# Kernel tuning notes

Hardware: AMD Instinct MI355X
Metric: run time of the kernel (lower is better)

Reference implementation:

```python
import jax, jax.numpy as jnp
import numpy as np

B, N = 2048, 110
H1, F1 = 5, 24   # gat1: 5 heads, 24-dim, concat
H2, F2 = 3, 3    # gat2: 3 heads, 3-dim, average
NEG = -9e15
ALPHA = 0.2  # tf.nn.leaky_relu default alpha


def _glorot(key, shape):
    fan_in, fan_out = shape[-2], shape[-1]
    lim = np.sqrt(6.0 / (fan_in + fan_out))
    return jax.random.uniform(key, shape, jnp.float32, -lim, lim)


def setup_inputs() -> dict:
    key = jax.random.key(0)
    ks = jax.random.split(key, 12)
    X = jax.random.normal(ks[0], (B, N, N), jnp.float32)
    # sparse-ish 0/1 adjacency with self-loops
    A = (jax.random.uniform(ks[1], (B, N, N)) < 0.3).astype(jnp.float32)
    A = jnp.maximum(A, jnp.eye(N, dtype=jnp.float32)[None])
    return {
        "X": X,
        "A": A,
        "M": jax.random.normal(ks[2], (N, N), jnp.float32),  # learnable mask
        "W1": _glorot(ks[3], (H1, N, F1)),
        "as1": _glorot(ks[4], (H1, F1, 1))[..., 0],
        "an1": _glorot(ks[5], (H1, F1, 1))[..., 0],
        "b1": jnp.zeros((F1,), jnp.float32),
        "W2": _glorot(ks[6], (H2, H1 * F1, F2)),
        "as2": _glorot(ks[7], (H2, F2, 1))[..., 0],
        "an2": _glorot(ks[8], (H2, F2, 1))[..., 0],
        "b2": jnp.zeros((F2,), jnp.float32),
        "fc1_w": _glorot(ks[9], (F2, 1)),
        "fc2_w": _glorot(ks[10], (N, N)),
    }


def _gat_layer(X, A, W, a_s, a_n, b, concat):
    # X: [B,N,Din]; W: [H,Din,F]; a_s,a_n: [H,F]; b: [F]
    feats = jnp.einsum('bni,hif->bhnf', X, W)               # per-head projection
    e_s = jnp.einsum('bhnf,hf->bhn', feats, a_s)
    e_n = jnp.einsum('bhnf,hf->bhn', feats, a_n)
    e = jax.nn.leaky_relu(e_s[..., :, None] + e_n[..., None, :], ALPHA)  # [B,H,N,N]
    e = jnp.where(A[:, None] > 0.0, e, NEG)                  # adjacency mask
    attn = jax.nn.softmax(e, axis=-1)
    h = jnp.einsum('bhnm,bhmf->bhnf', attn, feats) + b       # aggregate + bias
    if concat:
        h = jax.nn.leaky_relu(h, ALPHA)
        b_, hh, n_, f_ = h.shape
        return h.transpose(0, 2, 1, 3).reshape(b_, n_, hh * f_)
    # 'average': add heads / H, then activation
    return jax.nn.leaky_relu(h.mean(axis=1), ALPHA)


def reference(X, A, M, W1, as1, an1, b1, W2, as2, an2, b2, fc1_w, fc2_w):
    Xm = X * jax.nn.sigmoid(M)[None]                         # learnable mask gating
    h1 = _gat_layer(Xm, A, W1, as1, an1, b1, concat=True)    # [B,N,H1*F1]
    h2 = _gat_layer(h1, A, W2, as2, an2, b2, concat=False)   # [B,N,F2]
    node_prob = jax.nn.sigmoid(h2 @ fc1_w)                   # [B,N,1]
    t = node_prob.reshape(-1, N)                             # [B,N]
    attn_prob = jax.nn.softmax(t @ fc2_w, axis=-1)           # [B,N]
    return jnp.sum(t * attn_prob, axis=1, keepdims=True)     # [B,1]
```

## Files before the change

kernel.cpp:

```cpp
#include <hip/hip_runtime.h>
#include <math.h>

#define NB 2048
#define NV 110
#define NH1 5
#define NF1 24
#define NH2 3
#define NF2 3
#define C1 (NH1*NF1)
#define LALPHA 0.2f

constexpr int NN = NV*NV;
constexpr int T1 = 512;
constexpr int KP = 136;
constexpr int W1ROWS = 144;

typedef _Float16 f16;
typedef f16  f16x8 __attribute__((ext_vector_type(8)));
typedef f16  f16x4 __attribute__((ext_vector_type(4)));
typedef __fp16 h16x2 __attribute__((ext_vector_type(2)));
typedef float f32x4 __attribute__((ext_vector_type(4)));

__device__ __forceinline__ f32x4 mfma16(f16x8 a, f16x8 b, f32x4 c) {
  return __builtin_amdgcn_mfma_f32_16x16x32_f16(a, b, c, 0, 0, 0);
}
__device__ __forceinline__ float lrelu(float x){ return x > 0.f ? x : LALPHA*x; }
__device__ __forceinline__ float frcp(float x){ return __builtin_amdgcn_rcpf(x); }
__device__ __forceinline__ float sigm(float x){ return frcp(1.f+__expf(-x)); }
__device__ __forceinline__ float expm4(float v){
  return __builtin_amdgcn_exp2f(fmaf(v, 1.442695041f, -5.770780163f));
}
__device__ __forceinline__ float wmax(float v){
  #pragma unroll
  for (int d=32; d; d>>=1) v = fmaxf(v, __shfl_xor(v,d));
  return v;
}
__device__ __forceinline__ float wsum(float v){
  #pragma unroll
  for (int d=32; d; d>>=1) v += __shfl_xor(v,d);
  return v;
}
__device__ __forceinline__ f32x4 ld4u(const float* p){
  f32x4 v; __builtin_memcpy(&v, p, 16); return v;
}

__global__ void precomp_kernel(const float* __restrict__ M, const float* __restrict__ W1,
                               const float* __restrict__ as1, const float* __restrict__ an1,
                               const float* __restrict__ W2, const float* __restrict__ as2,
                               const float* __restrict__ an2, const float* __restrict__ fc2w,
                               float* __restrict__ Msig, f16* __restrict__ W1tg,
                               f16* __restrict__ W2tg, f16* __restrict__ fc2tg) {
  const int i = blockIdx.x*256 + threadIdx.x;
  if (i < NN) {
    Msig[i] = sigm(M[i]);
  } else if (i < NN + W1ROWS*KP) {
    const int j = i - NN, f = j/KP, k = j%KP;
    float v = 0.f;
    if (k < NV) {
      if (f < C1) {
        v = W1[(f/NF1)*(NV*NF1) + k*NF1 + (f%NF1)];
      } else if (f >= 128 && f < 133) {
        const int h = f - 128;
        for (int ff = 0; ff < NF1; ++ff)
          v += W1[h*(NV*NF1) + k*NF1 + ff] * as1[h*NF1 + ff];
      } else if (f >= 133 && f < 138) {
        const int h = f - 133;
        for (int ff = 0; ff < NF1; ++ff)
          v += W1[h*(NV*NF1) + k*NF1 + ff] * an1[h*NF1 + ff];
      }
    }
    W1tg[f*KP + k] = (f16)v;
  } else if (i < NN + W1ROWS*KP + 16*KP) {
    const int j = i - NN - W1ROWS*KP, r = j/KP, k = j%KP;
    float v = 0.f;
    if (k < C1) {
      if (r < 9) {
        v = W2[(r/NF2)*(C1*NF2) + k*NF2 + (r%NF2)];
      } else if (r < 12) {
        const int g = r - 9;
        for (int f2 = 0; f2 < NF2; ++f2)
          v += W2[g*(C1*NF2) + k*NF2 + f2] * as2[g*NF2 + f2];
      } else if (r < 15) {
        const int g = r - 12;
        for (int f2 = 0; f2 < NF2; ++f2)
          v += W2[g*(C1*NF2) + k*NF2 + f2] * an2[g*NF2 + f2];
      }
    }
    W2tg[r*KP + k] = (f16)v;
  } else if (i < NN + W1ROWS*KP + 16*KP + 112*KP) {
    const int j = i - NN - W1ROWS*KP - 16*KP, col = j/KP, k = j%KP;
    float v = 0.f;
    if (col < NV && k < NV) v = fc2w[k*NV + col];
    fc2tg[col*KP + k] = (f16)v;
  }
}

__global__ __launch_bounds__(T1, 4) void gat_fused(
  const float* __restrict__ X, const float* __restrict__ A,
  const float* __restrict__ Msig, const f16* __restrict__ W1tg,
  const float* __restrict__ b1,  const f16* __restrict__ W2tg,
  const float* __restrict__ b2,  const float* __restrict__ fc1w,
  const f16* __restrict__ fc2tg, float* __restrict__ out)
{
  __shared__ __attribute__((aligned(16))) f16 sXm [112*KP];
  __shared__ __attribute__((aligned(16))) f16 sFt [128*KP];
  __shared__ __attribute__((aligned(16))) f16 sF2t[16*KP];
  __shared__ __attribute__((aligned(16))) float sES [NH1*112];
  __shared__ __attribute__((aligned(16))) float sEN [NH1*128];
  __shared__ __attribute__((aligned(16))) float sES2[NH2*112];
  __shared__ __attribute__((aligned(16))) float sEN2[NH2*128];
  __shared__ unsigned long long sAM[2*112];
  __shared__ __attribute__((aligned(16))) float sROW [112];
  __shared__ __attribute__((aligned(16))) float sROW2[3*112];

  const int b = blockIdx.x, tid = threadIdx.x;
  const int wv = tid >> 6, lane = tid & 63;
  const int lr = lane & 15, lh = lane >> 4;
  const float* __restrict__ Xb = X + (size_t)b*NN;
  const float* __restrict__ Ab = A + (size_t)b*NN;

  float* const sT = sES;
  float* const sS = sES + 112;
  f16*   const t16 = sF2t;

  for (int n = tid; n < 110; n += T1) {
    *(unsigned*)&sXm[n*KP + 110] = 0u;
    *(uint4*)&sXm[n*KP + 112] = uint4{0,0,0,0};
    *(uint4*)&sXm[n*KP + 120] = uint4{0,0,0,0};
    *(uint4*)&sXm[n*KP + 128] = uint4{0,0,0,0};
  }
  for (int i = tid; i < 2*KP/8; i += T1)
    ((uint4*)&sXm[110*KP])[i] = uint4{0,0,0,0};
  for (int n = tid; n < 128; n += T1) {
    *(uint4*)&sFt[n*KP + 112] = uint4{0,0,0,0};
    *(uint4*)&sFt[n*KP + 120] = uint4{0,0,0,0};
    *(uint4*)&sFt[n*KP + 128] = uint4{0,0,0,0};
  }
  for (int i = tid; i < (16*KP)/8; i += T1)
    ((uint4*)sF2t)[i] = uint4{0,0,0,0};
  if (tid < 4) sAM[220 + tid] = 0ull;

  for (int t = tid; t < NV*28; t += T1) {
    const int n = t/28, c = t%28, k = 4*c;
    if (c < 27) {
      f32x4 x = ld4u(Xb + n*NV + k);
      f32x4 m = ld4u(Msig + n*NV + k);
      union { f16x4 v4; h16x2 h2[2]; } u;
      u.h2[0] = __builtin_amdgcn_cvt_pkrtz(x[0]*m[0], x[1]*m[1]);
      u.h2[1] = __builtin_amdgcn_cvt_pkrtz(x[2]*m[2], x[3]*m[3]);
      *(f16x4*)&sXm[n*KP + k] = u.v4;
    } else {
      sXm[n*KP + 108] = (f16)(Xb[n*NV+108]*Msig[n*NV+108]);
      sXm[n*KP + 109] = (f16)(Xb[n*NV+109]*Msig[n*NV+109]);
    }
  }
  #pragma unroll
  for (int i = 0; i < 14; ++i) {
    const int n = wv + 8*i;
    if (n < NV) {
      unsigned long long m0 = __ballot(Ab[n*NV + lane] > 0.f);
      const int mm = 64 + lane;
      unsigned long long m1 = __ballot((mm < NV) && (Ab[n*NV + mm] > 0.f));
      if (lane == 0) { sAM[2*n] = m0; sAM[2*n+1] = m1; }
    }
  }
  f16x8 bW[4], bL[4];
  #pragma unroll
  for (int k = 0; k < 4; ++k)
    bW[k] = *(const f16x8*)&W1tg[(wv*16 + lr)*KP + k*32 + lh*8];
  if (wv < 2) {
    #pragma unroll
    for (int k = 0; k < 4; ++k)
      bL[k] = *(const f16x8*)&W1tg[(128 + lr)*KP + k*32 + lh*8];
  }
  __syncthreads();

  #pragma unroll
  for (int m = 0; m < 7; ++m) {
    f32x4 acc = {0.f,0.f,0.f,0.f};
    #pragma unroll
    for (int k = 0; k < 4; ++k) {
      f16x8 af = *(const f16x8*)&sXm[(m*16 + lr)*KP + k*32 + lh*8];
      acc = mfma16(af, bW[k], acc);
    }
    f16x4 v;
    #pragma unroll
    for (int r = 0; r < 4; ++r) v[r] = (f16)acc[r];
    *(f16x4*)&sFt[(wv*16 + lr)*KP + m*16 + lh*4] = v;
  }
  if (wv < 2) {
    const int mlo = wv ? 4 : 0, mhi = wv ? 7 : 4;
    for (int m = mlo; m < mhi; ++m) {
      f32x4 acc = {0.f,0.f,0.f,0.f};
      #pragma unroll
      for (int k = 0; k < 4; ++k) {
        f16x8 af = *(const f16x8*)&sXm[(m*16 + lr)*KP + k*32 + lh*8];
        acc = mfma16(af, bL[k], acc);
      }
      const int mg0 = m*16 + lh*4;
      if (lr < 5)       *(f32x4*)&sES[lr*112 + mg0] = acc;
      else if (lr < 10) *(f32x4*)&sEN[(lr-5)*128 + mg0] = acc;
    }
  }
  __syncthreads();

  const int row  = wv*16 + lr;
  const int arow = (row < 112) ? row : 0;
  const unsigned long long am0 = sAM[2*arow], am1 = sAM[2*arow+1];
  const float bvt0 = (lr < NF1) ? b1[lr] : 0.f;
  const float bvt1 = (16 + lr < NF1) ? b1[16 + lr] : 0.f;

  f16 h1r[5][2][4];
  f16x8 pa[4];
  if (wv < 7) {
    #pragma unroll
    for (int p = 0; p < 5; ++p) {
      const float es = sES[p*112 + row];
      float psum = 0.f;
      #pragma unroll
      for (int k = 0; k < 4; ++k) {
        const int cb = k*32 + lh*8;
        const f32x4 enA = *(const f32x4*)&sEN[p*128 + cb];
        const f32x4 enB = *(const f32x4*)&sEN[p*128 + cb + 4];
        const unsigned bits = (unsigned)(((cb & 64) ? am1 : am0) >> (cb & 63)) & 0xFFu;
        float e[8];
        #pragma unroll
        for (int j = 0; j < 8; ++j) {
          float v = es + ((j < 4) ? enA[j] : enB[j-4]);
          v = fmaxf(v, LALPHA*v);
          v = (bits & (1u << j)) ? v : -1e30f;
          e[j] = expm4(v);
          psum += e[j];
        }
        union { f16x8 v8; h16x2 h2[4]; } u;
        u.h2[0] = __builtin_amdgcn_cvt_pkrtz(e[0], e[1]);
        u.h2[1] = __builtin_amdgcn_cvt_pkrtz(e[2], e[3]);
        u.h2[2] = __builtin_amdgcn_cvt_pkrtz(e[4], e[5]);
        u.h2[3] = __builtin_amdgcn_cvt_pkrtz(e[6], e[7]);
        pa[k] = u.v8;
      }
      psum += __shfl_xor(psum, 16);
      psum += __shfl_xor(psum, 32);
      if (lh == 0) sROW[row] = psum;
      #pragma unroll
      for (int nt2 = 0; nt2 < 2; ++nt2) {
        f32x4 acc = {0.f,0.f,0.f,0.f};
        #pragma unroll
        for (int k = 0; k < 4; ++k) {
          f16x8 bf = *(const f16x8*)&sFt[(p*NF1 + nt2*16 + lr)*KP + k*32 + lh*8];
          acc = mfma16(pa[k], bf, acc);
        }
        const f32x4 rs = *(const f32x4*)&sROW[wv*16 + lh*4];
        const float bv = nt2 ? bvt1 : bvt0;
        #pragma unroll
        for (int r = 0; r < 4; ++r)
          h1r[p][nt2][r] = (f16)lrelu(acc[r]*frcp(rs[r]) + bv);
      }
    }
    #pragma unroll
    for (int p = 0; p < 5; ++p) {
      #pragma unroll
      for (int nt2 = 0; nt2 < 2; ++nt2) {
        const int fl = nt2*16 + lr;
        if (fl < NF1) {
          #pragma unroll
          for (int r = 0; r < 4; ++r) {
            const int mg = wv*16 + lh*4 + r;
            if (mg < NV) sXm[mg*KP + p*NF1 + fl] = h1r[p][nt2][r];
          }
        }
      }
    }
    {
      f32x4 acc = {0.f,0.f,0.f,0.f};
      #pragma unroll
      for (int k = 0; k < 4; ++k) {
        f16x8 af = *(const f16x8*)&sXm[(wv*16 + lr)*KP + k*32 + lh*8];
        f16x8 bf = *(const f16x8*)&W2tg[lr*KP + k*32 + lh*8];
        acc = mfma16(af, bf, acc);
      }
      const int mg0 = wv*16 + lh*4;
      if (lr < 9) {
        #pragma unroll
        for (int r = 0; r < 4; ++r) {
          const int mg = mg0 + r;
          if (mg < NV) sF2t[lr*KP + mg] = (f16)acc[r];
        }
      } else if (lr < 12) {
        *(f32x4*)&sES2[(lr-9)*112 + mg0] = acc;
      } else if (lr < 15) {
        *(f32x4*)&sEN2[(lr-12)*128 + mg0] = acc;
      }
    }
  }
  __syncthreads();

  f32x4 a2_0 = {0.f,0.f,0.f,0.f};
  f32x4 a2_1 = {0.f,0.f,0.f,0.f};
  f32x4 a2_2 = {0.f,0.f,0.f,0.f};
  if (wv < 7) {
    #pragma unroll
    for (int g = 0; g < 3; ++g) {
      const float es = sES2[g*112 + row];
      float psum = 0.f;
      #pragma unroll
      for (int k = 0; k < 4; ++k) {
        const int cb = k*32 + lh*8;
        const f32x4 enA = *(const f32x4*)&sEN2[g*128 + cb];
        const f32x4 enB = *(const f32x4*)&sEN2[g*128 + cb + 4];
        const unsigned bits = (unsigned)(((cb & 64) ? am1 : am0) >> (cb & 63)) & 0xFFu;
        float e[8];
        #pragma unroll
        for (int j = 0; j < 8; ++j) {
          float v = es + ((j < 4) ? enA[j] : enB[j-4]);
          v = fmaxf(v, LALPHA*v);
          v = (bits & (1u << j)) ? v : -1e30f;
          e[j] = expm4(v);
          psum += e[j];
        }
        union { f16x8 v8; h16x2 h2[4]; } u;
        u.h2[0] = __builtin_amdgcn_cvt_pkrtz(e[0], e[1]);
        u.h2[1] = __builtin_amdgcn_cvt_pkrtz(e[2], e[3]);
        u.h2[2] = __builtin_amdgcn_cvt_pkrtz(e[4], e[5]);
        u.h2[3] = __builtin_amdgcn_cvt_pkrtz(e[6], e[7]);
        pa[k] = u.v8;
      }
      psum += __shfl_xor(psum, 16);
      psum += __shfl_xor(psum, 32);
      if (lh == 0) sROW2[g*112 + row] = psum;
      const int brow = (lr < NF2) ? (g*NF2 + lr) : 15;
      #pragma unroll
      for (int k = 0; k < 4; ++k) {
        f16x8 bf = *(const f16x8*)&sF2t[brow*KP + k*32 + lh*8];
        if (g == 0)      a2_0 = mfma16(pa[k], bf, a2_0);
        else if (g == 1) a2_1 = mfma16(pa[k], bf, a2_1);
        else             a2_2 = mfma16(pa[k], bf, a2_2);
      }
    }
    const int mg0 = wv*16 + lh*4;
    const float fcv = (lr < NF2) ? fc1w[lr] : 0.f;
    const float b2v = (lr < NF2) ? b2[lr]  : 0.f;
    const f32x4 rs0 = *(const f32x4*)&sROW2[0*112 + mg0];
    const f32x4 rs1 = *(const f32x4*)&sROW2[1*112 + mg0];
    const f32x4 rs2 = *(const f32x4*)&sROW2[2*112 + mg0];
    #pragma unroll
    for (int r = 0; r < 4; ++r) {
      const float hsum = a2_0[r]*frcp(rs0[r]) + a2_1[r]*frcp(rs1[r])
                       + a2_2[r]*frcp(rs2[r]);
      float hv = (lr < NF2) ? lrelu(hsum*(1.f/NH2) + b2v)*fcv : 0.f;
      hv += __shfl_xor(hv, 1);
      hv += __shfl_xor(hv, 2);
      hv += __shfl_xor(hv, 4);
      hv += __shfl_xor(hv, 8);
      if (lr == 0) {
        const int mg = mg0 + r;
        if (mg < NV) sT[mg] = sigm(hv);
      }
    }
  }
  __syncthreads();
  for (int i = tid; i < 16*KP; i += T1) {
    const int k = i % KP;
    t16[i] = (k < NV) ? (f16)sT[k] : (f16)0.f;
  }
  __syncthreads();
  if (wv < 7) {
    f32x4 acc = {0.f,0.f,0.f,0.f};
    #pragma unroll
    for (int k = 0; k < 4; ++k) {
      f16x8 af = *(const f16x8*)&t16[lr*KP + k*32 + lh*8];
      f16x8 bf = *(const f16x8*)&fc2tg[(wv*16 + lr)*KP + k*32 + lh*8];
      acc = mfma16(af, bf, acc);
    }
    const int col = wv*16 + lr;
    if (lh == 0 && col < NV) sS[col] = acc[0];
  }
  __syncthreads();
  if (wv == 0) {
    const float s0 = sS[lane];
    const float s1 = (64+lane < NV) ? sS[64+lane] : -1e38f;
    const float mx = wmax(fmaxf(s0, s1));
    const float p0 = __expf(s0 - mx);
    const float p1 = (64+lane < NV) ? __expf(s1 - mx) : 0.f;
    const float sum = wsum(p0 + p1);
    float val = sT[lane]*p0 + ((64+lane < NV) ? sT[64+lane]*p1 : 0.f);
    val = wsum(val);
    if (lane == 0) out[b] = val*frcp(sum);
  }
}

extern "C" void kernel_launch(void* const* d_in, const int* in_sizes, int n_in,
                              void* d_out, int out_size, void* d_ws, size_t ws_size,
                              hipStream_t stream) {
  const float* X   = (const float*)d_in[0];
  const float* A   = (const float*)d_in[1];
  const float* M   = (const float*)d_in[2];
  const float* W1  = (const float*)d_in[3];
  const float* as1 = (const float*)d_in[4];
  const float* an1 = (const float*)d_in[5];
  const float* b1  = (const float*)d_in[6];
  const float* W2  = (const float*)d_in[7];
  const float* as2 = (const float*)d_in[8];
  const float* an2 = (const float*)d_in[9];
  const float* b2  = (const float*)d_in[10];
  const float* fc1 = (const float*)d_in[11];
  const float* fc2 = (const float*)d_in[12];
  float* out = (float*)d_out;

  float* Msig = (float*)d_ws;
  f16* W1tg  = (f16*)((char*)d_ws + 48400);
  f16* W2tg  = (f16*)((char*)d_ws + 48400 + W1ROWS*KP*2);
  f16* fc2tg = (f16*)((char*)d_ws + 48400 + W1ROWS*KP*2 + 16*KP*2);

  const int pre_items = NN + W1ROWS*KP + 16*KP + 112*KP;
  precomp_kernel<<<(pre_items + 255)/256, 256, 0, stream>>>(
      M, W1, as1, an1, W2, as2, an2, fc2, Msig, W1tg, W2tg, fc2tg);
  gat_fused<<<NB, T1, 0, stream>>>(X, A, Msig, W1tg, b1, W2tg,
                                   b2, fc1, fc2tg, out);
}
```

Before: 148.8 us.

## Make GAT kernel persistent and prefetch next batch's inputs during layer 2

Launches a fixed grid of 512 blocks that each loop over four graphs instead of one block per graph. Staging of the next graph's X and adjacency into shared memory is moved after layer-1 completes, so its global loads overlap the layer-2 attention and final readout. The attention-logit projection is also spread across seven waves instead of two, and per-block constants are hoisted out of the loop. This trades fewer resident blocks and possibly less latency hiding across blocks for reuse of setup work and overlap of loads with compute.

```diff
diff --git a/kernel.cpp b/kernel.cpp
--- a/kernel.cpp
+++ b/kernel.cpp
@@ -12,6 +12,8 @@
 
 constexpr int NN = NV*NV;
 constexpr int T1 = 512;
+constexpr int GRID = 512;
+constexpr int ITERS = NB/GRID;
 constexpr int KP = 136;
 constexpr int W1ROWS = 144;
 
@@ -113,15 +115,42 @@
   __shared__ __attribute__((aligned(16))) float sROW [112];
   __shared__ __attribute__((aligned(16))) float sROW2[3*112];
 
-  const int b = blockIdx.x, tid = threadIdx.x;
+  const int tid = threadIdx.x;
   const int wv = tid >> 6, lane = tid & 63;
   const int lr = lane & 15, lh = lane >> 4;
-  const float* __restrict__ Xb = X + (size_t)b*NN;
-  const float* __restrict__ Ab = A + (size_t)b*NN;
 
   float* const sT = sES;
   float* const sS = sES + 112;
   f16*   const t16 = sF2t;
+
+  auto stage_xm = [&](const float* __restrict__ Xb) {
+    for (int t = tid; t < NV*28; t += T1) {
+      const int n = t/28, c = t%28, k = 4*c;
+      if (c < 27) {
+        f32x4 x = ld4u(Xb + n*NV + k);
+        f32x4 m = ld4u(Msig + n*NV + k);
+        union { f16x4 v4; h16x2 h2[2]; } u;
+        u.h2[0] = __builtin_amdgcn_cvt_pkrtz(x[0]*m[0], x[1]*m[1]);
+        u.h2[1] = __builtin_amdgcn_cvt_pkrtz(x[2]*m[2], x[3]*m[3]);
+        *(f16x4*)&sXm[n*KP + k] = u.v4;
+      } else {
+        sXm[n*KP + 108] = (f16)(Xb[n*NV+108]*Msig[n*NV+108]);
+        sXm[n*KP + 109] = (f16)(Xb[n*NV+109]*Msig[n*NV+109]);
+      }
+    }
+  };
+  auto stage_am = [&](const float* __restrict__ Ab) {
+    #pragma unroll
+    for (int i = 0; i < 14; ++i) {
+      const int n = wv + 8*i;
+      if (n < NV) {
+        unsigned long long m0 = __ballot(Ab[n*NV + lane] > 0.f);
+        const int mm = 64 + lane;
+        unsigned long long m1 = __ballot((mm < NV) && (Ab[n*NV + mm] > 0.f));
+        if (lane == 0) { sAM[2*n] = m0; sAM[2*n+1] = m1; }
+      }
+    }
+  };
 
   for (int n = tid; n < 110; n += T1) {
     *(unsigned*)&sXm[n*KP + 110] = 0u;
@@ -140,252 +169,248 @@
     ((uint4*)sF2t)[i] = uint4{0,0,0,0};
   if (tid < 4) sAM[220 + tid] = 0ull;
 
-  for (int t = tid; t < NV*28; t += T1) {
-    const int n = t/28, c = t%28, k = 4*c;
-    if (c < 27) {
-      f32x4 x = ld4u(Xb + n*NV + k);
-      f32x4 m = ld4u(Msig + n*NV + k);
-      union { f16x4 v4; h16x2 h2[2]; } u;
-      u.h2[0] = __builtin_amdgcn_cvt_pkrtz(x[0]*m[0], x[1]*m[1]);
-      u.h2[1] = __builtin_amdgcn_cvt_pkrtz(x[2]*m[2], x[3]*m[3]);
-      *(f16x4*)&sXm[n*KP + k] = u.v4;
-    } else {
-      sXm[n*KP + 108] = (f16)(Xb[n*NV+108]*Msig[n*NV+108]);
-      sXm[n*KP + 109] = (f16)(Xb[n*NV+109]*Msig[n*NV+109]);
-    }
-  }
-  #pragma unroll
-  for (int i = 0; i < 14; ++i) {
-    const int n = wv + 8*i;
-    if (n < NV) {
-      unsigned long long m0 = __ballot(Ab[n*NV + lane] > 0.f);
-      const int mm = 64 + lane;
-      unsigned long long m1 = __ballot((mm < NV) && (Ab[n*NV + mm] > 0.f));
-      if (lane == 0) { sAM[2*n] = m0; sAM[2*n+1] = m1; }
-    }
-  }
+  stage_xm(X + (size_t)blockIdx.x*NN);
+  stage_am(A + (size_t)blockIdx.x*NN);
+
   f16x8 bW[4], bL[4];
   #pragma unroll
   for (int k = 0; k < 4; ++k)
     bW[k] = *(const f16x8*)&W1tg[(wv*16 + lr)*KP + k*32 + lh*8];
-  if (wv < 2) {
+  if (wv < 7) {
     #pragma unroll
     for (int k = 0; k < 4; ++k)
       bL[k] = *(const f16x8*)&W1tg[(128 + lr)*KP + k*32 + lh*8];
   }
-  __syncthreads();
-
-  #pragma unroll
-  for (int m = 0; m < 7; ++m) {
-    f32x4 acc = {0.f,0.f,0.f,0.f};
+
+  const float bvt0 = (lr < NF1) ? b1[lr] : 0.f;
+  const float bvt1 = (16 + lr < NF1) ? b1[16 + lr] : 0.f;
+  const float fcv  = (lr < NF2) ? fc1w[lr] : 0.f;
+  const float b2v  = (lr < NF2) ? b2[lr]  : 0.f;
+
+  #pragma unroll 1
+  for (int it = 0; it < ITERS; ++it) {
+    const int bi = it*GRID + blockIdx.x;
+    __syncthreads();
+
     #pragma unroll
-    for (int k = 0; k < 4; ++k) {
-      f16x8 af = *(const f16x8*)&sXm[(m*16 + lr)*KP + k*32 + lh*8];
-      acc = mfma16(af, bW[k], acc);
-    }
-    f16x4 v;
-    #pragma unroll
-    for (int r = 0; r < 4; ++r) v[r] = (f16)acc[r];
-    *(f16x4*)&sFt[(wv*16 + lr)*KP + m*16 + lh*4] = v;
-  }
-  if (wv < 2) {
-    const int mlo = wv ? 4 : 0, mhi = wv ? 7 : 4;
-    for (int m = mlo; m < mhi; ++m) {
+    for (int m = 0; m < 7; ++m) {
       f32x4 acc = {0.f,0.f,0.f,0.f};
       #pragma unroll
       for (int k = 0; k < 4; ++k) {
         f16x8 af = *(const f16x8*)&sXm[(m*16 + lr)*KP + k*32 + lh*8];
+        acc = mfma16(af, bW[k], acc);
+      }
+      f16x4 v;
+      #pragma unroll
+      for (int r = 0; r < 4; ++r) v[r] = (f16)acc[r];
+      *(f16x4*)&sFt[(wv*16 + lr)*KP + m*16 + lh*4] = v;
+    }
+    if (wv < 7) {
+      f32x4 acc = {0.f,0.f,0.f,0.f};
+      #pragma unroll
+      for (int k = 0; k < 4; ++k) {
+        f16x8 af = *(const f16x8*)&sXm[(wv*16 + lr)*KP + k*32 + lh*8];
         acc = mfma16(af, bL[k], acc);
       }
-      const int mg0 = m*16 + lh*4;
+      const int mg0 = wv*16 + lh*4;
       if (lr < 5)       *(f32x4*)&sES[lr*112 + mg0] = acc;
       else if (lr < 10) *(f32x4*)&sEN[(lr-5)*128 + mg0] = acc;
     }
-  }
-  __syncthreads();
-
-  const int row  = wv*16 + lr;
-  const int arow = (row < 112) ? row : 0;
-  const unsigned long long am0 = sAM[2*arow], am1 = sAM[2*arow+1];
-  const float bvt0 = (lr < NF1) ? b1[lr] : 0.f;
-  const float bvt1 = (16 + lr < NF1) ? b1[16 + lr] : 0.f;
-
-  f16 h1r[5][2][4];
-  f16x8 pa[4];
-  if (wv < 7) {
+    __syncthreads();
+
+    const int row  = wv*16 + lr;
+    const int arow = (row < 112) ? row : 0;
+    const unsigned long long am0 = sAM[2*arow], am1 = sAM[2*arow+1];
+
+    f16x8 bW2[4];
     #pragma unroll
-    for (int p = 0; p < 5; ++p) {
-      const float es = sES[p*112 + row];
-      float psum = 0.f;
-      #pragma unroll
-      for (int k = 0; k < 4; ++k) {
-        const int cb = k*32 + lh*8;
-        const f32x4 enA = *(const f32x4*)&sEN[p*128 + cb];
-        const f32x4 enB = *(const f32x4*)&sEN[p*128 + cb + 4];
-        const unsigned bits = (unsigned)(((cb & 64) ? am1 : am0) >> (cb & 63)) & 0xFFu;
-        float e[8];
-        #pragma unroll
-        for (int j = 0; j < 8; ++j) {
-          float v = es + ((j < 4) ? enA[j] : enB[j-4]);
-          v = fmaxf(v, LALPHA*v);
-          v = (bits & (1u << j)) ? v : -1e30f;
-          e[j] = expm4(v);
-          psum += e[j];
-        }
-        union { f16x8 v8; h16x2 h2[4]; } u;
-        u.h2[0] = __builtin_amdgcn_cvt_pkrtz(e[0], e[1]);
-        u.h2[1] = __builtin_amdgcn_cvt_pkrtz(e[2], e[3]);
-        u.h2[2] = __builtin_amdgcn_cvt_pkrtz(e[4], e[5]);
-        u.h2[3] = __builtin_amdgcn_cvt_pkrtz(e[6], e[7]);
-        pa[k] = u.v8;
-      }
-      psum += __shfl_xor(psum, 16);
-      psum += __shfl_xor(psum, 32);
-      if (lh == 0) sROW[row] = psum;
-      #pragma unroll
-      for (int nt2 = 0; nt2 < 2; ++nt2) {
+    for (int k = 0; k < 4; ++k)
+      bW2[k] = *(const f16x8*)&W2tg[lr*KP + k*32 + lh*8];
+
+    f16 h1r[5][2][4];
+    f16x8 pa[4];
+    if (wv < 7) {
+      #pragma unroll
+      for (int p = 0; p < 5; ++p) {
+        const float es = sES[p*112 + row];
+        float psum = 0.f;
+        #pragma unroll
+        for (int k = 0; k < 4; ++k) {
+          const int cb = k*32 + lh*8;
+          const f32x4 enA = *(const f32x4*)&sEN[p*128 + cb];
+          const f32x4 enB = *(const f32x4*)&sEN[p*128 + cb + 4];
+          const unsigned bits = (unsigned)(((cb & 64) ? am1 : am0) >> (cb & 63)) & 0xFFu;
+          float e[8];
+          #pragma unroll
+          for (int j = 0; j < 8; ++j) {
+            float v = es + ((j < 4) ? enA[j] : enB[j-4]);
+            v = fmaxf(v, LALPHA*v);
+            v = (bits & (1u << j)) ? v : -1e30f;
+            e[j] = expm4(v);
+            psum += e[j];
+          }
+          union { f16x8 v8; h16x2 h2[4]; } u;
+          u.h2[0] = __builtin_amdgcn_cvt_pkrtz(e[0], e[1]);
+          u.h2[1] = __builtin_amdgcn_cvt_pkrtz(e[2], e[3]);
+          u.h2[2] = __builtin_amdgcn_cvt_pkrtz(e[4], e[5]);
+          u.h2[3] = __builtin_amdgcn_cvt_pkrtz(e[6], e[7]);
+          pa[k] = u.v8;
+        }
+        psum += __shfl_xor(psum, 16);
+        psum += __shfl_xor(psum, 32);
+        if (lh == 0) sROW[row] = psum;
+        #pragma unroll
+        for (int nt2 = 0; nt2 < 2; ++nt2) {
+          f32x4 acc = {0.f,0.f,0.f,0.f};
+          #pragma unroll
+          for (int k = 0; k < 4; ++k) {
+            f16x8 bf = *(const f16x8*)&sFt[(p*NF1 + nt2*16 + lr)*KP + k*32 + lh*8];
+            acc = mfma16(pa[k], bf, acc);
+          }
+          const f32x4 rs = *(const f32x4*)&sROW[wv*16 + lh*4];
+          const float bv = nt2 ? bvt1 : bvt0;
+          #pragma unroll
+          for (int r = 0; r < 4; ++r)
+            h1r[p][nt2][r] = (f16)lrelu(acc[r]*frcp(rs[r]) + bv);
+        }
+      }
+      #pragma unroll
+      for (int p = 0; p < 5; ++p) {
+        #pragma unroll
+        for (int nt2 = 0; nt2 < 2; ++nt2) {
+          const int fl = nt2*16 + lr;
+          if (fl < NF1) {
+            #pragma unroll
+            for (int r = 0; r < 4; ++r) {
+              const int mg = wv*16 + lh*4 + r;
+              if (mg < NV) sXm[mg*KP + p*NF1 + fl] = h1r[p][nt2][r];
+            }
+          }
+        }
+      }
+      {
         f32x4 acc = {0.f,0.f,0.f,0.f};
         #pragma unroll
         for (int k = 0; k < 4; ++k) {
-          f16x8 bf = *(const f16x8*)&sFt[(p*NF1 + nt2*16 + lr)*KP + k*32 + lh*8];
-          acc = mfma16(pa[k], bf, acc);
-        }
-        const f32x4 rs = *(const f32x4*)&sROW[wv*16 + lh*4];
-        const float bv = nt2 ? bvt1 : bvt0;
-        #pragma unroll
-        for (int r = 0; r < 4; ++r)
-          h1r[p][nt2][r] = (f16)lrelu(acc[r]*frcp(rs[r]) + bv);
-      }
-    }
-    #pragma unroll
-    for (int p = 0; p < 5; ++p) {
-      #pragma unroll
-      for (int nt2 = 0; nt2 < 2; ++nt2) {
-        const int fl = nt2*16 + lr;
-        if (fl < NF1) {
+          f16x8 af = *(const f16x8*)&sXm[(wv*16 + lr)*KP + k*32 + lh*8];
+          acc = mfma16(af, bW2[k], acc);
+        }
+        const int mg0 = wv*16 + lh*4;
+        if (lr < 9) {
           #pragma unroll
           for (int r = 0; r < 4; ++r) {
-            const int mg = wv*16 + lh*4 + r;
-            if (mg < NV) sXm[mg*KP + p*NF1 + fl] = h1r[p][nt2][r];
+            const int mg = mg0 + r;
+            if (mg < NV) sF2t[lr*KP + mg] = (f16)acc[r];
           }
-        }
-      }
-    }
-    {
+        } else if (lr < 12) {
+          *(f32x4*)&sES2[(lr-9)*112 + mg0] = acc;
+        } else if (lr < 15) {
+          *(f32x4*)&sEN2[(lr-12)*128 + mg0] = acc;
+        }
+      }
+    }
+    __syncthreads();
+
+    if (it + 1 < ITERS) {
+      for (int n = tid; n < 110; n += T1) {
+        *(unsigned*)&sXm[n*KP + 110] = 0u;
+        *(uint4*)&sXm[n*KP + 112] = uint4{0,0,0,0};
+        *(uint4*)&sXm[n*KP + 120] = uint4{0,0,0,0};
+      }
+      stage_xm(X + (size_t)(bi + GRID)*NN);
+      stage_am(A + (size_t)(bi + GRID)*NN);
+    }
+
+    f32x4 a2_0 = {0.f,0.f,0.f,0.f};
+    f32x4 a2_1 = {0.f,0.f,0.f,0.f};
+    f32x4 a2_2 = {0.f,0.f,0.f,0.f};
+    if (wv < 7) {
+      #pragma unroll
+      for (int g = 0; g < 3; ++g) {
+        const float es = sES2[g*112 + row];
+        float psum = 0.f;
+        #pragma unroll
+        for (int k = 0; k < 4; ++k) {
+          const int cb = k*32 + lh*8;
+          const f32x4 enA = *(const f32x4*)&sEN2[g*128 + cb];
+          const f32x4 enB = *(const f32x4*)&sEN2[g*128 + cb + 4];
+          const unsigned bits = (unsigned)(((cb & 64) ? am1 : am0) >> (cb & 63)) & 0xFFu;
+          float e[8];
+          #pragma unroll
+          for (int j = 0; j < 8; ++j) {
+            float v = es + ((j < 4) ? enA[j] : enB[j-4]);
+            v = fmaxf(v, LALPHA*v);
+            v = (bits & (1u << j)) ? v : -1e30f;
+            e[j] = expm4(v);
+            psum += e[j];
+          }
+          union { f16x8 v8; h16x2 h2[4]; } u;
+          u.h2[0] = __builtin_amdgcn_cvt_pkrtz(e[0], e[1]);
+          u.h2[1] = __builtin_amdgcn_cvt_pkrtz(e[2], e[3]);
+          u.h2[2] = __builtin_amdgcn_cvt_pkrtz(e[4], e[5]);
+          u.h2[3] = __builtin_amdgcn_cvt_pkrtz(e[6], e[7]);
+          pa[k] = u.v8;
+        }
+        psum += __shfl_xor(psum, 16);
+        psum += __shfl_xor(psum, 32);
+        if (lh == 0) sROW2[g*112 + row] = psum;
+        const int brow = (lr < NF2) ? (g*NF2 + lr) : 15;
+        #pragma unroll
+        for (int k = 0; k < 4; ++k) {
+          f16x8 bf = *(const f16x8*)&sF2t[brow*KP + k*32 + lh*8];
+          if (g == 0)      a2_0 = mfma16(pa[k], bf, a2_0);
+          else if (g == 1) a2_1 = mfma16(pa[k], bf, a2_1);
+          else             a2_2 = mfma16(pa[k], bf, a2_2);
+        }
+      }
+      const int mg0 = wv*16 + lh*4;
+      const f32x4 rs0 = *(const f32x4*)&sROW2[0*112 + mg0];
+      const f32x4 rs1 = *(const f32x4*)&sROW2[1*112 + mg0];
+      const f32x4 rs2 = *(const f32x4*)&sROW2[2*112 + mg0];
+      #pragma unroll
+      for (int r = 0; r < 4; ++r) {
+        const float hsum = a2_0[r]*frcp(rs0[r]) + a2_1[r]*frcp(rs1[r])
+                         + a2_2[r]*frcp(rs2[r]);
+        float hv = (lr < NF2) ? lrelu(hsum*(1.f/NH2) + b2v)*fcv : 0.f;
+        hv += __shfl_xor(hv, 1);
+        hv += __shfl_xor(hv, 2);
+        hv += __shfl_xor(hv, 4);
+        hv += __shfl_xor(hv, 8);
+        if (lr == 0) {
+          const int mg = mg0 + r;
+          if (mg < NV) sT[mg] = sigm(hv);
+        }
+      }
+    }
+    __syncthreads();
+    for (int i = tid; i < 16*KP; i += T1) {
+      const int k = i % KP;
+      t16[i] = (k < NV) ? (f16)sT[k] : (f16)0.f;
+    }
+    __syncthreads();
+    if (wv < 7) {
       f32x4 acc = {0.f,0.f,0.f,0.f};
       #pragma unroll
       for (int k = 0; k < 4; ++k) {
-        f16x8 af = *(const f16x8*)&sXm[(wv*16 + lr)*KP + k*32 + lh*8];
-        f16x8 bf = *(const f16x8*)&W2tg[lr*KP + k*32 + lh*8];
+        f16x8 af = *(const f16x8*)&t16[lr*KP + k*32 + lh*8];
+        f16x8 bf = *(const f16x8*)&fc2tg[(wv*16 + lr)*KP + k*32 + lh*8];
         acc = mfma16(af, bf, acc);
       }
-      const int mg0 = wv*16 + lh*4;
-      if (lr < 9) {
-        #pragma unroll
-        for (int r = 0; r < 4; ++r) {
-          const int mg = mg0 + r;
-          if (mg < NV) sF2t[lr*KP + mg] = (f16)acc[r];
-        }
-      } else if (lr < 12) {
-        *(f32x4*)&sES2[(lr-9)*112 + mg0] = acc;
-      } else if (lr < 15) {
-        *(f32x4*)&sEN2[(lr-12)*128 + mg0] = acc;
-      }
-    }
-  }
-  __syncthreads();
-
-  f32x4 a2_0 = {0.f,0.f,0.f,0.f};
-  f32x4 a2_1 = {0.f,0.f,0.f,0.f};
-  f32x4 a2_2 = {0.f,0.f,0.f,0.f};
-  if (wv < 7) {
-    #pragma unroll
-    for (int g = 0; g < 3; ++g) {
-      const float es = sES2[g*112 + row];
-      float psum = 0.f;
-      #pragma unroll
-      for (int k = 0; k < 4; ++k) {
-        const int cb = k*32 + lh*8;
-        const f32x4 enA = *(const f32x4*)&sEN2[g*128 + cb];
-        const f32x4 enB = *(const f32x4*)&sEN2[g*128 + cb + 4];
-        const unsigned bits = (unsigned)(((cb & 64) ? am1 : am0) >> (cb & 63)) & 0xFFu;
-        float e[8];
-        #pragma unroll
-        for (int j = 0; j < 8; ++j) {
-          float v = es + ((j < 4) ? enA[j] : enB[j-4]);
-          v = fmaxf(v, LALPHA*v);
-          v = (bits & (1u << j)) ? v : -1e30f;
-          e[j] = expm4(v);
-          psum += e[j];
-        }
-        union { f16x8 v8; h16x2 h2[4]; } u;
-        u.h2[0] = __builtin_amdgcn_cvt_pkrtz(e[0], e[1]);
-        u.h2[1] = __builtin_amdgcn_cvt_pkrtz(e[2], e[3]);
-        u.h2[2] = __builtin_amdgcn_cvt_pkrtz(e[4], e[5]);
-        u.h2[3] = __builtin_amdgcn_cvt_pkrtz(e[6], e[7]);
-        pa[k] = u.v8;
-      }
-      psum += __shfl_xor(psum, 16);
-      psum += __shfl_xor(psum, 32);
-      if (lh == 0) sROW2[g*112 + row] = psum;
-      const int brow = (lr < NF2) ? (g*NF2 + lr) : 15;
-      #pragma unroll
-      for (int k = 0; k < 4; ++k) {
-        f16x8 bf = *(const f16x8*)&sF2t[brow*KP + k*32 + lh*8];
-        if (g == 0)      a2_0 = mfma16(pa[k], bf, a2_0);
-        else if (g == 1) a2_1 = mfma16(pa[k], bf, a2_1);
-        else             a2_2 = mfma16(pa[k], bf, a2_2);
-      }
-    }
-    const int mg0 = wv*16 + lh*4;
-    const float fcv = (lr < NF2) ? fc1w[lr] : 0.f;
-    const float b2v = (lr < NF2) ? b2[lr]  : 0.f;
-    const f32x4 rs0 = *(const f32x4*)&sROW2[0*112 + mg0];
-    const f32x4 rs1 = *(const f32x4*)&sROW2[1*112 + mg0];
-    const f32x4 rs2 = *(const f32x4*)&sROW2[2*112 + mg0];
-    #pragma unroll
-    for (int r = 0; r < 4; ++r) {
-      const float hsum = a2_0[r]*frcp(rs0[r]) + a2_1[r]*frcp(rs1[r])
-                       + a2_2[r]*frcp(rs2[r]);
-      float hv = (lr < NF2) ? lrelu(hsum*(1.f/NH2) + b2v)*fcv : 0.f;
-      hv += __shfl_xor(hv, 1);
-      hv += __shfl_xor(hv, 2);
-      hv += __shfl_xor(hv, 4);
-      hv += __shfl_xor(hv, 8);
-      if (lr == 0) {
-        const int mg = mg0 + r;
-        if (mg < NV) sT[mg] = sigm(hv);
-      }
-    }
-  }
-  __syncthreads();
-  for (int i = tid; i < 16*KP; i += T1) {
-    const int k = i % KP;
-    t16[i] = (k < NV) ? (f16)sT[k] : (f16)0.f;
-  }
-  __syncthreads();
-  if (wv < 7) {
-    f32x4 acc = {0.f,0.f,0.f,0.f};
-    #pragma unroll
-    for (int k = 0; k < 4; ++k) {
-      f16x8 af = *(const f16x8*)&t16[lr*KP + k*32 + lh*8];
-      f16x8 bf = *(const f16x8*)&fc2tg[(wv*16 + lr)*KP + k*32 + lh*8];
-      acc = mfma16(af, bf, acc);
-    }
-    const int col = wv*16 + lr;
-    if (lh == 0 && col < NV) sS[col] = acc[0];
-  }
-  __syncthreads();
-  if (wv == 0) {
-    const float s0 = sS[lane];
-    const float s1 = (64+lane < NV) ? sS[64+lane] : -1e38f;
-    const float mx = wmax(fmaxf(s0, s1));
-    const float p0 = __expf(s0 - mx);
-    const float p1 = (64+lane < NV) ? __expf(s1 - mx) : 0.f;
-    const float sum = wsum(p0 + p1);
-    float val = sT[lane]*p0 + ((64+lane < NV) ? sT[64+lane]*p1 : 0.f);
-    val = wsum(val);
-    if (lane == 0) out[b] = val*frcp(sum);
+      const int col = wv*16 + lr;
+      if (lh == 0 && col < NV) sS[col] = acc[0];
+    }
+    __syncthreads();
+    if (wv == 0) {
+      const float s0 = sS[lane];
+      const float s1 = (64+lane < NV) ? sS[64+lane] : -1e38f;
+      const float mx = wmax(fmaxf(s0, s1));
+      const float p0 = __expf(s0 - mx);
+      const float p1 = (64+lane < NV) ? __expf(s1 - mx) : 0.f;
+      const float sum = wsum(p0 + p1);
+      float val = sT[lane]*p0 + ((64+lane < NV) ? sT[64+lane]*p1 : 0.f);
+      val = wsum(val);
+      if (lane == 0) out[bi] = val*frcp(sum);
+    }
   }
 }
 
@@ -415,6 +440,6 @@
   const int pre_items = NN + W1ROWS*KP + 16*KP + 112*KP;
   precomp_kernel<<<(pre_items + 255)/256, 256, 0, stream>>>(
       M, W1, as1, an1, W2, as2, an2, fc2, Msig, W1tg, W2tg, fc2tg);
-  gat_fused<<<NB, T1, 0, stream>>>(X, A, Msig, W1tg, b1, W2tg,
-                                   b2, fc1, fc2tg, out);
-}
+  gat_fused<<<GRID, T1, 0, stream>>>(X, A, Msig, W1tg, b1, W2tg,
+                                     b2, fc1, fc2tg, out);
+}
```

Result: slower. 280.7 us (+88.6%).
